# Kernel tuning notes

Hardware: AMD Instinct MI355X
Metric: run time of the kernel (lower is better)

## Reference

```python
import jax, jax.numpy as jnp
import numpy as np
import math

S, W, H = 256, 128, 768   # sentence, word, hidden (hidden fixed to 768 by PositionalEncoding)
TOPK = 3                  # len(inputs) > 2 branch: fuse 3 nearest sentences


def positional_encoding(length, d_model):
    # Standard sinusoidal PE, identical to the torch buffer construction.
    pos = jnp.arange(length, dtype=jnp.float32)[:, None]                      # [L,1]
    div = jnp.exp(jnp.arange(0, d_model, 2, dtype=jnp.float32)
                  * (-math.log(10000.0) / d_model))                           # [H/2]
    pe = jnp.zeros((length, d_model), dtype=jnp.float32)
    pe = pe.at[:, 0::2].set(jnp.sin(pos * div))
    pe = pe.at[:, 1::2].set(jnp.cos(pos * div))
    return pe


def setup_inputs() -> dict:
    key = jax.random.key(0)
    inputs = jax.random.normal(key, (S, W, H), dtype=jnp.float32)
    return {"inputs": inputs}


def reference(inputs):
    s, w, h = inputs.shape
    # Pairwise L1 distance between the FIRST word vector of each sentence
    # (matmulCell only ever sees x[i,0,:] and k[0,j,:] == inputs[j,0,:]).
    x0 = inputs[:, 0, :]                                                      # [S,H]
    dist = jnp.sum(jnp.abs(x0[:, None, :] - x0[None, :, :]), axis=-1)         # [S,S]
    # torch.sort ascending -> 3 nearest sentences (self included, dist 0)
    idx = jnp.argsort(dist, axis=1)[:, :TOPK]                                 # [S,3] int
    fused = inputs[idx].reshape(s, TOPK * w, h)                               # [S,3W,H]
    # Positional encoding added to both q/v stream and k stream (same tensor;
    # dropout p=0.1 is identity in eval mode).
    x = fused + positional_encoding(TOPK * w, h)[None]                        # [S,3W,H]
    # Scaled dot-product self-attention per row.
    scores = jnp.einsum('slh,smh->slm', x, x) / jnp.sqrt(jnp.float32(h))      # [S,3W,3W]
    attn = jax.nn.softmax(scores, axis=-1)
    out = jnp.einsum('slm,smh->slh', attn, x)                                 # [S,3W,H]
    # D_Attention keeps only the first word-1 rows of each fused output.
    return out[:, :w - 1, :]                                                  # [S,W-1,H]
```

## Files before the change

kernel.cpp:

```cpp
#include <hip/hip_runtime.h>

#define NS 256
#define NW 128
#define NH 768
#define NL 384
#define WH (NW*NH)
#define OUTROWS 127

typedef __attribute__((ext_vector_type(8))) short short8;
typedef __attribute__((ext_vector_type(8))) unsigned short ushort8;
typedef __attribute__((ext_vector_type(4))) float f32x4;

#define XS_STRIDE 72
#define PS_STRIDE 392
#define SMEM_PS   (NL*XS_STRIDE*2)
#define SMEM_RED  (SMEM_PS + 128*PS_STRIDE*2)
#define SMEM_TOTAL (SMEM_RED + 4096)

__device__ __forceinline__ unsigned short bf16b(float f) {
  union { float f; unsigned u; } x; x.f = f;
  return (unsigned short)((x.u + 0x7fffu + ((x.u >> 16) & 1u)) >> 16);
}
__device__ __forceinline__ float b2f(unsigned short h) {
  union { unsigned u; float f; } x; x.u = ((unsigned)h) << 16;
  return x.f;
}

__global__ __launch_bounds__(256) void k_x0t(const float* __restrict__ inp,
                                             float* __restrict__ x0T) {
  int gid = blockIdx.x * 256 + threadIdx.x;
  int h = gid >> 8, i = gid & 255;
  x0T[h * NS + i] = inp[(size_t)i * WH + h];
}

__global__ __launch_bounds__(256) void k_top3(const float* __restrict__ inp,
                                              const float* __restrict__ x0T,
                                              int* __restrict__ idxw) {
  const int i = blockIdx.x, t = threadIdx.x;
  __shared__ float xi[NH];
  __shared__ float part[4][NS];
  __shared__ float dist[NS];
  for (int h = t; h < NH; h += 256) xi[h] = inp[(size_t)i * WH + h];
  __syncthreads();
  const int j4 = (t & 63) * 4;
  const int hq = t >> 6;
  float s0 = 0.f, s1 = 0.f, s2 = 0.f, s3 = 0.f;
  const int hbeg = hq * 192, hend = hbeg + 192;
  for (int h = hbeg; h < hend; ++h) {
    float4 v = *(const float4*)&x0T[h * NS + j4];
    float q = xi[h];
    s0 += fabsf(q - v.x); s1 += fabsf(q - v.y);
    s2 += fabsf(q - v.z); s3 += fabsf(q - v.w);
  }
  part[hq][j4 + 0] = s0; part[hq][j4 + 1] = s1;
  part[hq][j4 + 2] = s2; part[hq][j4 + 3] = s3;
  __syncthreads();
  dist[t] = part[0][t] + part[1][t] + part[2][t] + part[3][t];
  __syncthreads();
  if (t == 0) {
    #pragma unroll
    for (int k = 0; k < 3; ++k) {
      float best = 3.4e38f; int bj = 0;
      for (int j = 0; j < NS; ++j)
        if (dist[j] < best) { best = dist[j]; bj = j; }
      idxw[i * 3 + k] = bj;
      dist[bj] = 3.4e38f;
    }
  }
}

__global__ __launch_bounds__(256) void k_pe(unsigned short* __restrict__ peb) {
  int gid = blockIdx.x * 256 + threadIdx.x;
  if (gid >= NL * NH) return;
  int l = gid / NH, d = gid - l * NH;
  const float c = -0.011992630687355995f;
  float dv = __expf((float)(d & ~1) * c);
  float ang = (float)l * dv;
  float v = (d & 1) ? cosf(ang) : sinf(ang);
  peb[gid] = bf16b(v);
}

__global__ __launch_bounds__(256) void k_inpb(const float* __restrict__ inp,
                                              unsigned short* __restrict__ inpb) {
  size_t gid = (size_t)blockIdx.x * 256 + threadIdx.x;
  size_t base = gid * 8;
  float4 a = *(const float4*)(inp + base);
  float4 b = *(const float4*)(inp + base + 4);
  ushort8 o;
  o[0] = bf16b(a.x); o[1] = bf16b(a.y); o[2] = bf16b(a.z); o[3] = bf16b(a.w);
  o[4] = bf16b(b.x); o[5] = bf16b(b.y); o[6] = bf16b(b.z); o[7] = bf16b(b.w);
  *(ushort8*)(inpb + base) = o;
}

template<bool BF>
__device__ __forceinline__ void load8(const void* __restrict__ src, size_t off, float* v) {
  if constexpr (BF) {
    ushort8 u = *reinterpret_cast<const ushort8*>((const unsigned short*)src + off);
    #pragma unroll
    for (int j = 0; j < 8; ++j) v[j] = b2f(u[j]);
  } else {
    float4 a = *reinterpret_cast<const float4*>((const float*)src + off);
    float4 b = *reinterpret_cast<const float4*>((const float*)src + off + 4);
    v[0] = a.x; v[1] = a.y; v[2] = a.z; v[3] = a.w;
    v[4] = b.x; v[5] = b.y; v[6] = b.z; v[7] = b.w;
  }
}

template<bool BF>
__global__ __launch_bounds__(512)
void k_attn(const void* __restrict__ xsrc, const unsigned short* __restrict__ peb,
            const int* __restrict__ idxw, float* __restrict__ out) {
  extern __shared__ char smem[];
  unsigned short* Xs = (unsigned short*)smem;
  unsigned short* Ps = (unsigned short*)(smem + SMEM_PS);
  float* red1 = (float*)(smem + SMEM_RED);
  float* red2 = red1 + 512;

  const int s = blockIdx.x;
  const int tid = threadIdx.x;
  const int lane = tid & 63, wid = tid >> 6;
  const int lrow = lane & 15, lhi = lane >> 4;
  const int i0 = idxw[s * 3 + 0], i1 = idxw[s * 3 + 1], i2 = idxw[s * 3 + 2];

  const f32x4 fz = {0.f, 0.f, 0.f, 0.f};
  f32x4 acc[4][6];
  #pragma unroll
  for (int qs = 0; qs < 4; ++qs)
    #pragma unroll
    for (int kf = 0; kf < 6; ++kf) acc[qs][kf] = fz;

  const int qh = wid & 1, kq = wid >> 1;

  for (int hc = 0; hc < 12; ++hc) {
    const int h0 = hc * 64;
    #pragma unroll
    for (int it = 0; it < 6; ++it) {
      const int p = tid + it * 512;
      const int r = p >> 3, c8 = (p & 7) * 8;
      const int src = (r < 128) ? i0 : (r < 256 ? i1 : i2);
      float xv[8], pv[8];
      load8<BF>(xsrc, (size_t)src * WH + (size_t)(r & 127) * NH + h0 + c8, xv);
      load8<true>(peb, (size_t)r * NH + h0 + c8, pv);
      ushort8 o;
      #pragma unroll
      for (int j = 0; j < 8; ++j) o[j] = bf16b(xv[j] + pv[j]);
      *reinterpret_cast<ushort8*>(&Xs[r * XS_STRIDE + c8]) = o;
    }
    __syncthreads();
    #pragma unroll
    for (int ks = 0; ks < 64; ks += 32) {
      short8 a[4];
      #pragma unroll
      for (int qs = 0; qs < 4; ++qs)
        a[qs] = *reinterpret_cast<const short8*>(&Xs[(qh * 64 + qs * 16 + lrow) * XS_STRIDE + ks + lhi * 8]);
      #pragma unroll
      for (int kf = 0; kf < 6; ++kf) {
        short8 b = *reinterpret_cast<const short8*>(&Xs[(kq * 96 + kf * 16 + lrow) * XS_STRIDE + ks + lhi * 8]);
        #pragma unroll
        for (int qs = 0; qs < 4; ++qs)
          acc[qs][kf] = __builtin_amdgcn_mfma_f32_16x16x32_bf16(a[qs], b, acc[qs][kf], 0, 0, 0);
      }
    }
    __syncthreads();
  }

  const float scale = 0.03608439182435161f;
  float mx[4][4];
  #pragma unroll
  for (int qs = 0; qs < 4; ++qs)
    #pragma unroll
    for (int r = 0; r < 4; ++r) {
      float m = acc[qs][0][r];
      #pragma unroll
      for (int kf = 1; kf < 6; ++kf) m = fmaxf(m, acc[qs][kf][r]);
      #pragma unroll
      for (int d = 1; d < 16; d <<= 1) m = fmaxf(m, __shfl_xor(m, d, 64));
      mx[qs][r] = m;
    }
  if (lrow == 0) {
    #pragma unroll
    for (int qs = 0; qs < 4; ++qs)
      #pragma unroll
      for (int r = 0; r < 4; ++r)
        red1[(qh * 64 + qs * 16 + lhi * 4 + r) * 4 + kq] = mx[qs][r];
  }
  __syncthreads();
  float sm[4][4];
  #pragma unroll
  for (int qs = 0; qs < 4; ++qs)
    #pragma unroll
    for (int r = 0; r < 4; ++r) {
      const int row = qh * 64 + qs * 16 + lhi * 4 + r;
      mx[qs][r] = fmaxf(fmaxf(red1[row * 4 + 0], red1[row * 4 + 1]),
                        fmaxf(red1[row * 4 + 2], red1[row * 4 + 3]));
      sm[qs][r] = 0.f;
    }
  #pragma unroll
  for (int qs = 0; qs < 4; ++qs)
    #pragma unroll
    for (int kf = 0; kf < 6; ++kf)
      #pragma unroll
      for (int r = 0; r < 4; ++r) {
        float p = __expf((acc[qs][kf][r] - mx[qs][r]) * scale);
        acc[qs][kf][r] = p;
        sm[qs][r] += p;
      }
  #pragma unroll
  for (int qs = 0; qs < 4; ++qs)
    #pragma unroll
    for (int r = 0; r < 4; ++r) {
      #pragma unroll
      for (int d = 1; d < 16; d <<= 1) sm[qs][r] += __shfl_xor(sm[qs][r], d, 64);
    }
  if (lrow == 0) {
    #pragma unroll
    for (int qs = 0; qs < 4; ++qs)
      #pragma unroll
      for (int r = 0; r < 4; ++r)
        red2[(qh * 64 + qs * 16 + lhi * 4 + r) * 4 + kq] = sm[qs][r];
  }
  __syncthreads();
  #pragma unroll
  for (int qs = 0; qs < 4; ++qs)
    #pragma unroll
    for (int r = 0; r < 4; ++r) {
      const int row = qh * 64 + qs * 16 + lhi * 4 + r;
      float t = red2[row * 4 + 0] + red2[row * 4 + 1] + red2[row * 4 + 2] + red2[row * 4 + 3];
      sm[qs][r] = 1.0f / t;
    }
  #pragma unroll
  for (int qs = 0; qs < 4; ++qs)
    #pragma unroll
    for (int kf = 0; kf < 6; ++kf)
      #pragma unroll
      for (int r = 0; r < 4; ++r)
        Ps[(qh * 64 + qs * 16 + lhi * 4 + r) * PS_STRIDE + kq * 96 + kf * 16 + lrow] =
            bf16b(acc[qs][kf][r] * sm[qs][r]);
  __syncthreads();

  const int qb = wid & 3, hh = wid >> 2;
  short8 pa[2][12];
  #pragma unroll
  for (int qs = 0; qs < 2; ++qs)
    #pragma unroll
    for (int m0 = 0; m0 < 12; ++m0)
      pa[qs][m0] = *reinterpret_cast<const short8*>(&Ps[(qb * 32 + qs * 16 + lrow) * PS_STRIDE + m0 * 32 + lhi * 8]);

  unsigned short* VT = Xs;
  for (int t4 = 0; t4 < 12; ++t4) {
    const int h0 = t4 * 64;
    #pragma unroll
    for (int it = 0; it < 6; ++it) {
      const int p = tid + it * 512;
      const int m = p >> 3, c8 = (p & 7) * 8;
      const int src = (m < 128) ? i0 : (m < 256 ? i1 : i2);
      float xv[8], pv[8];
      load8<BF>(xsrc, (size_t)src * WH + (size_t)(m & 127) * NH + h0 + c8, xv);
      load8<true>(peb, (size_t)m * NH + h0 + c8, pv);
      #pragma unroll
      for (int j = 0; j < 8; ++j)
        VT[(c8 + j) * PS_STRIDE + m] = bf16b(xv[j] + pv[j]);
    }
    __syncthreads();
    f32x4 o00 = fz, o01 = fz, o10 = fz, o11 = fz;
    #pragma unroll
    for (int m0 = 0; m0 < 12; ++m0) {
      short8 b0 = *reinterpret_cast<const short8*>(&VT[(hh * 32 + lrow) * PS_STRIDE + m0 * 32 + lhi * 8]);
      short8 b1 = *reinterpret_cast<const short8*>(&VT[(hh * 32 + 16 + lrow) * PS_STRIDE + m0 * 32 + lhi * 8]);
      o00 = __builtin_amdgcn_mfma_f32_16x16x32_bf16(pa[0][m0], b0, o00, 0, 0, 0);
      o01 = __builtin_amdgcn_mfma_f32_16x16x32_bf16(pa[0][m0], b1, o01, 0, 0, 0);
      o10 = __builtin_amdgcn_mfma_f32_16x16x32_bf16(pa[1][m0], b0, o10, 0, 0, 0);
      o11 = __builtin_amdgcn_mfma_f32_16x16x32_bf16(pa[1][m0], b1, o11, 0, 0, 0);
    }
    #pragma unroll
    for (int qs = 0; qs < 2; ++qs)
      #pragma unroll
      for (int hf = 0; hf < 2; ++hf) {
        f32x4 o = (qs == 0) ? (hf == 0 ? o00 : o01) : (hf == 0 ? o10 : o11);
        #pragma unroll
        for (int r = 0; r < 4; ++r) {
          const int q = qb * 32 + qs * 16 + lhi * 4 + r;
          if (q < OUTROWS)
            out[(size_t)s * (OUTROWS * NH) + (size_t)q * NH + h0 + hh * 32 + hf * 16 + lrow] = o[r];
        }
      }
    __syncthreads();
  }
}

extern "C" void kernel_launch(void* const* d_in, const int* in_sizes, int n_in,
                              void* d_out, int out_size, void* d_ws, size_t ws_size,
                              hipStream_t stream) {
  (void)in_sizes; (void)n_in; (void)out_size;
  const float* inp = (const float*)d_in[0];
  float* out = (float*)d_out;
  char* ws = (char*)d_ws;

  float* x0T          = (float*)ws;
  unsigned short* peb = (unsigned short*)(ws + 786432);
  int* idxw           = (int*)(ws + 1376256);
  unsigned short* inpb= (unsigned short*)(ws + 1379328);
  const bool primary = ws_size >= (size_t)51710976;

  hipLaunchKernelGGL(k_x0t, dim3(768), dim3(256), 0, stream, inp, x0T);
  hipLaunchKernelGGL(k_top3, dim3(256), dim3(256), 0, stream, inp, x0T, idxw);
  hipLaunchKernelGGL(k_pe, dim3(1152), dim3(256), 0, stream, peb);

  if (primary) {
    hipLaunchKernelGGL(k_inpb, dim3(12288), dim3(256), 0, stream, inp, inpb);
    hipFuncSetAttribute((const void*)k_attn<true>,
                        hipFuncAttributeMaxDynamicSharedMemorySize, SMEM_TOTAL);
    hipLaunchKernelGGL(k_attn<true>, dim3(256), dim3(512), SMEM_TOTAL, stream,
                       (const void*)inpb, peb, idxw, out);
  } else {
    hipFuncSetAttribute((const void*)k_attn<false>,
                        hipFuncAttributeMaxDynamicSharedMemorySize, SMEM_TOTAL);
    hipLaunchKernelGGL(k_attn<false>, dim3(256), dim3(512), SMEM_TOTAL, stream,
                       (const void*)inp, peb, idxw, out);
  }
}
```

Baseline: 158.0 us.

## Fuse top-3 distance kernel, drop transpose, swizzle VT smem writes

Removes the separate x0 transpose kernel. k_top3 now runs with 1024 threads, reading rows directly, reducing with wavefront shuffles, and picking the argmin via packed 64-bit keys instead of a serial scan. The V-transpose shared-memory store and the matching reads use an XOR swizzle to cut bank conflicts. The staging index mapping is restructured so the source row is chosen per iteration rather than per element. Together these aim to cut launch overhead, the serial top-k time and LDS conflicts.

Result: faster. 138.9 us (-12.1%).

```diff
diff --git a/kernel.cpp b/kernel.cpp
--- a/kernel.cpp
+++ b/kernel.cpp
@@ -26,46 +26,46 @@
   return x.f;
 }
 
-__global__ __launch_bounds__(256) void k_x0t(const float* __restrict__ inp,
-                                             float* __restrict__ x0T) {
-  int gid = blockIdx.x * 256 + threadIdx.x;
-  int h = gid >> 8, i = gid & 255;
-  x0T[h * NS + i] = inp[(size_t)i * WH + h];
-}
-
-__global__ __launch_bounds__(256) void k_top3(const float* __restrict__ inp,
-                                              const float* __restrict__ x0T,
-                                              int* __restrict__ idxw) {
+__global__ __launch_bounds__(1024) void k_top3(const float* __restrict__ inp,
+                                               int* __restrict__ idxw) {
   const int i = blockIdx.x, t = threadIdx.x;
-  __shared__ float xi[NH];
-  __shared__ float part[4][NS];
+  __shared__ float xi[772];
   __shared__ float dist[NS];
-  for (int h = t; h < NH; h += 256) xi[h] = inp[(size_t)i * WH + h];
-  __syncthreads();
-  const int j4 = (t & 63) * 4;
-  const int hq = t >> 6;
-  float s0 = 0.f, s1 = 0.f, s2 = 0.f, s3 = 0.f;
-  const int hbeg = hq * 192, hend = hbeg + 192;
-  for (int h = hbeg; h < hend; ++h) {
-    float4 v = *(const float4*)&x0T[h * NS + j4];
-    float q = xi[h];
-    s0 += fabsf(q - v.x); s1 += fabsf(q - v.y);
-    s2 += fabsf(q - v.z); s3 += fabsf(q - v.w);
-  }
-  part[hq][j4 + 0] = s0; part[hq][j4 + 1] = s1;
-  part[hq][j4 + 2] = s2; part[hq][j4 + 3] = s3;
-  __syncthreads();
-  dist[t] = part[0][t] + part[1][t] + part[2][t] + part[3][t];
-  __syncthreads();
-  if (t == 0) {
-    #pragma unroll
-    for (int k = 0; k < 3; ++k) {
-      float best = 3.4e38f; int bj = 0;
-      for (int j = 0; j < NS; ++j)
-        if (dist[j] < best) { best = dist[j]; bj = j; }
+  __shared__ unsigned long long wkeys[16];
+  for (int h = t; h < NH; h += 1024) xi[h + h / 192] = inp[(size_t)i * WH + h];
+  __syncthreads();
+  const int c = t >> 2, seg = t & 3;
+  const float* __restrict__ row = inp + (size_t)c * WH + seg * 192;
+  const float* xis = xi + seg * 193;
+  float s = 0.f;
+  #pragma unroll 4
+  for (int h = 0; h < 192; h += 4) {
+    float4 v = *(const float4*)(row + h);
+    s += fabsf(xis[h]     - v.x) + fabsf(xis[h + 1] - v.y)
+       + fabsf(xis[h + 2] - v.z) + fabsf(xis[h + 3] - v.w);
+  }
+  s += __shfl_xor(s, 1, 64);
+  s += __shfl_xor(s, 2, 64);
+  if (seg == 0) dist[c] = s;
+  __syncthreads();
+  for (int k = 0; k < 3; ++k) {
+    float d = (t < NS) ? dist[t] : 3.4e38f;
+    unsigned long long key = ((unsigned long long)__float_as_uint(d) << 32) | (unsigned)t;
+    #pragma unroll
+    for (int dd = 1; dd < 64; dd <<= 1) {
+      unsigned long long o = __shfl_xor(key, dd, 64);
+      key = (o < key) ? o : key;
+    }
+    if ((t & 63) == 0) wkeys[t >> 6] = key;
+    __syncthreads();
+    if (t == 0) {
+      unsigned long long best = wkeys[0];
+      for (int w = 1; w < 16; ++w) if (wkeys[w] < best) best = wkeys[w];
+      int bj = (int)(best & 0xffffffffu);
       idxw[i * 3 + k] = bj;
       dist[bj] = 3.4e38f;
     }
+    __syncthreads();
   }
 }
 
@@ -135,11 +135,12 @@
     const int h0 = hc * 64;
     #pragma unroll
     for (int it = 0; it < 6; ++it) {
-      const int p = tid + it * 512;
-      const int r = p >> 3, c8 = (p & 7) * 8;
-      const int src = (r < 128) ? i0 : (r < 256 ? i1 : i2);
+      const int src = (it < 2) ? i0 : (it < 4 ? i1 : i2);
+      const int rl = (tid >> 3) + (it & 1) * 64;
+      const int r  = rl + (it >> 1) * 128;
+      const int c8 = (tid & 7) * 8;
       float xv[8], pv[8];
-      load8<BF>(xsrc, (size_t)src * WH + (size_t)(r & 127) * NH + h0 + c8, xv);
+      load8<BF>(xsrc, (size_t)src * WH + (size_t)rl * NH + h0 + c8, xv);
       load8<true>(peb, (size_t)r * NH + h0 + c8, pv);
       ushort8 o;
       #pragma unroll
@@ -251,22 +252,28 @@
     const int h0 = t4 * 64;
     #pragma unroll
     for (int it = 0; it < 6; ++it) {
-      const int p = tid + it * 512;
-      const int m = p >> 3, c8 = (p & 7) * 8;
-      const int src = (m < 128) ? i0 : (m < 256 ? i1 : i2);
+      const int src = (it < 2) ? i0 : (it < 4 ? i1 : i2);
+      const int ml = (tid >> 3) + (it & 1) * 64;
+      const int m  = ml + (it >> 1) * 128;
+      const int c8 = (tid & 7) * 8;
       float xv[8], pv[8];
-      load8<BF>(xsrc, (size_t)src * WH + (size_t)(m & 127) * NH + h0 + c8, xv);
+      load8<BF>(xsrc, (size_t)src * WH + (size_t)ml * NH + h0 + c8, xv);
       load8<true>(peb, (size_t)m * NH + h0 + c8, pv);
       #pragma unroll
-      for (int j = 0; j < 8; ++j)
-        VT[(c8 + j) * PS_STRIDE + m] = bf16b(xv[j] + pv[j]);
+      for (int j = 0; j < 8; ++j) {
+        const int vr = c8 + j;
+        VT[((vr * PS_STRIDE) + m) ^ (((vr >> 3) & 7) << 3)] = bf16b(xv[j] + pv[j]);
+      }
     }
     __syncthreads();
     f32x4 o00 = fz, o01 = fz, o10 = fz, o11 = fz;
     #pragma unroll
     for (int m0 = 0; m0 < 12; ++m0) {
-      short8 b0 = *reinterpret_cast<const short8*>(&VT[(hh * 32 + lrow) * PS_STRIDE + m0 * 32 + lhi * 8]);
-      short8 b1 = *reinterpret_cast<const short8*>(&VT[(hh * 32 + 16 + lrow) * PS_STRIDE + m0 * 32 + lhi * 8]);
+      const int vr0 = hh * 32 + lrow, vr1 = vr0 + 16;
+      short8 b0 = *reinterpret_cast<const short8*>(
+          &VT[((vr0 * PS_STRIDE) + m0 * 32 + lhi * 8) ^ (((vr0 >> 3) & 7) << 3)]);
+      short8 b1 = *reinterpret_cast<const short8*>(
+          &VT[((vr1 * PS_STRIDE) + m0 * 32 + lhi * 8) ^ (((vr1 >> 3) & 7) << 3)]);
       o00 = __builtin_amdgcn_mfma_f32_16x16x32_bf16(pa[0][m0], b0, o00, 0, 0, 0);
       o01 = __builtin_amdgcn_mfma_f32_16x16x32_bf16(pa[0][m0], b1, o01, 0, 0, 0);
       o10 = __builtin_amdgcn_mfma_f32_16x16x32_bf16(pa[1][m0], b0, o10, 0, 0, 0);
@@ -296,14 +303,12 @@
   float* out = (float*)d_out;
   char* ws = (char*)d_ws;
 
-  float* x0T          = (float*)ws;
-  unsigned short* peb = (unsigned short*)(ws + 786432);
-  int* idxw           = (int*)(ws + 1376256);
-  unsigned short* inpb= (unsigned short*)(ws + 1379328);
-  const bool primary = ws_size >= (size_t)51710976;
-
-  hipLaunchKernelGGL(k_x0t, dim3(768), dim3(256), 0, stream, inp, x0T);
-  hipLaunchKernelGGL(k_top3, dim3(256), dim3(256), 0, stream, inp, x0T, idxw);
+  unsigned short* peb = (unsigned short*)ws;
+  int* idxw           = (int*)(ws + 589824);
+  unsigned short* inpb= (unsigned short*)(ws + 592896);
+  const bool primary = ws_size >= (size_t)50924544;
+
+  hipLaunchKernelGGL(k_top3, dim3(256), dim3(1024), 0, stream, inp, idxw);
   hipLaunchKernelGGL(k_pe, dim3(1152), dim3(256), 0, stream, peb);
 
   if (primary) {
```
